# Kernel tuning notes

Hardware: AMD Instinct MI355X
Metric: run time of the kernel (lower is better)

## Reference

```python
import jax, jax.numpy as jnp
import numpy as np

B, T, D_IN, H, OUT = 512, 512, 64, 256, 64
EPS = 1e-5


def _ln(x, w, b):
    m = x.mean(-1, keepdims=True)
    v = ((x - m) ** 2).mean(-1, keepdims=True)
    return (x - m) / jnp.sqrt(v + EPS) * w + b


def _cell(x, h_prev, Wg, bg, gnw, gnb, Wc, bc, cnw, cnb):
    # LayerNormGRU cell
    combined = jnp.concatenate([x, h_prev], axis=-1)          # [B, D+H]
    rz = _ln(combined @ Wg.T + bg, gnw, gnb)                  # [B, 2H]
    r, z = jnp.split(rz, 2, axis=-1)
    r, z = jax.nn.sigmoid(r), jax.nn.sigmoid(z)
    combined_r = jnp.concatenate([x, r * h_prev], axis=-1)
    n = jnp.tanh(_ln(combined_r @ Wc.T + bc, cnw, cnb))       # [B, H]
    return (1.0 - z) * h_prev + z * n


def setup_inputs() -> dict:
    key = jax.random.key(0)
    ks = jax.random.split(key, 24)

    def uni(k, shape, fan_in):
        lim = 1.0 / np.sqrt(fan_in)
        return jax.random.uniform(k, shape, jnp.float32, -lim, lim)

    d0 = D_IN + H   # layer 0 cell input width
    d1 = H + H      # layer 1 cell input width
    return {
        "x": jax.random.normal(ks[0], (B, T, D_IN), jnp.float32),
        # layer 0
        "Wg0": uni(ks[1], (2 * H, d0), d0), "bg0": uni(ks[2], (2 * H,), d0),
        "gnw0": jnp.ones((2 * H,), jnp.float32), "gnb0": jnp.zeros((2 * H,), jnp.float32),
        "Wc0": uni(ks[3], (H, d0), d0), "bc0": uni(ks[4], (H,), d0),
        "cnw0": jnp.ones((H,), jnp.float32), "cnb0": jnp.zeros((H,), jnp.float32),
        # layer 1
        "Wg1": uni(ks[5], (2 * H, d1), d1), "bg1": uni(ks[6], (2 * H,), d1),
        "gnw1": jnp.ones((2 * H,), jnp.float32), "gnb1": jnp.zeros((2 * H,), jnp.float32),
        "Wc1": uni(ks[7], (H, d1), d1), "bc1": uni(ks[8], (H,), d1),
        "cnw1": jnp.ones((H,), jnp.float32), "cnb1": jnp.zeros((H,), jnp.float32),
        # output head
        "fcW": uni(ks[9], (OUT, H), H), "fcb": uni(ks[10], (OUT,), H),
    }


def reference(x, Wg0, bg0, gnw0, gnb0, Wc0, bc0, cnw0, cnb0,
              Wg1, bg1, gnw1, gnb1, Wc1, bc1, cnw1, cnb1, fcW, fcb):
    b = x.shape[0]
    h_init = (jnp.zeros((b, H), x.dtype), jnp.zeros((b, H), x.dtype))

    def step(carry, xt):
        h0, h1 = carry
        h0 = _cell(xt, h0, Wg0, bg0, gnw0, gnb0, Wc0, bc0, cnw0, cnb0)
        h1 = _cell(h0, h1, Wg1, bg1, gnw1, gnb1, Wc1, bc1, cnw1, cnb1)
        return (h0, h1), None

    (h0, h1), _ = jax.lax.scan(step, h_init, jnp.swapaxes(x, 0, 1))  # scan over T
    return h1 @ fcW.T + fcb  # [B, OUT]
```

## Files before the change

### kernel.cpp

```cpp
#include <hip/hip_runtime.h>


#define B_   512
#define T_   512
#define DIN  64
#define H_   256
#define OUT_ 64
#define EPS_ 1e-5f

typedef __attribute__((ext_vector_type(8))) short bf16x8;
typedef __attribute__((ext_vector_type(4))) float f32x4;

__device__ __forceinline__ unsigned short f2bf(float f) {
  unsigned int u = __float_as_uint(f);
  u += 0x7fffu + ((u >> 16) & 1u);
  return (unsigned short)(u >> 16);
}
__device__ __forceinline__ float bfh(unsigned short u) {
  return __uint_as_float(((unsigned int)u) << 16);
}
__device__ __forceinline__ float sigm_(float x) {
  return __builtin_amdgcn_rcpf(1.f + __expf(-x));
}
__device__ __forceinline__ float tanh_(float x) {
  return 1.f - 2.f * __builtin_amdgcn_rcpf(__expf(2.f * x) + 1.f);
}
template<int C>
__device__ __forceinline__ float dpp_add(float v) {
  int r = __builtin_amdgcn_update_dpp(0, __float_as_int(v), C, 0xF, 0xF, false);
  return v + __int_as_float(r);
}
__device__ __forceinline__ float red16(float v) {
  v = dpp_add<0x121>(v);
  v = dpp_add<0x122>(v);
  v = dpp_add<0x124>(v);
  v = dpp_add<0x128>(v);
  return v;
}

#define PIN8A(a) asm volatile("" : "+a"(a[0]), "+a"(a[1]), "+a"(a[2]), "+a"(a[3]), \
                                   "+a"(a[4]), "+a"(a[5]), "+a"(a[6]), "+a"(a[7]))

__global__ void prep_frag(const float* __restrict__ w, unsigned short* __restrict__ dst,
                          int N, int Ksrc, int koff) {
  int gid = blockIdx.x * 256 + threadIdx.x;
  if (gid >= N * 256) return;
  int n = gid >> 8, k = gid & 255;
  int idx = (((n >> 4) * 8 + (k >> 5)) * 64 + ((n & 15) + 16 * ((k >> 3) & 3))) * 8 + (k & 7);
  dst[idx] = f2bf(w[(size_t)n * Ksrc + koff + k]);
}

__global__ void prep_wx(const float* __restrict__ wg, const float* __restrict__ wc,
                        unsigned short* __restrict__ dst, int KX, int Kg, int Kc) {
  int gid = blockIdx.x * 256 + threadIdx.x;
  if (gid >= 768 * KX) return;
  int n = gid / KX, k = gid - n * KX;
  float v = (n < 512) ? wg[(size_t)n * Kg + k] : wc[(size_t)(n - 512) * Kc + k];
  dst[gid] = f2bf(v);
}

__global__ void bias_cat(const float* __restrict__ bg, const float* __restrict__ bc,
                         float* __restrict__ dst) {
  int i = blockIdx.x * 256 + threadIdx.x;
  if (i < 768) dst[i] = (i < 512) ? bg[i] : bc[i - 512];
}

__device__ __forceinline__ void precomp_tile(
    const void* __restrict__ Asrc, const unsigned short* __restrict__ wx,
    const float* __restrict__ bias, unsigned short* __restrict__ Pc,
    int TC, int t0, int KX, int AFP32,
    int mi, int nb, unsigned short* A_s, unsigned short* B_s, int t256)
{
  const int lane = t256 & 63, wv = t256 >> 6;
  const int m0 = mi * 128;
  const int bt = m0 / (TC * 16);
  const int tt0 = (m0 - bt * TC * 16) >> 4;
  const int mq = wv >> 1, nq = wv & 1;
  const int crow0 = (lane >> 4) * 4;

  f32x4 acc[4][4];
#pragma unroll
  for (int i = 0; i < 4; ++i)
#pragma unroll
    for (int j = 0; j < 4; ++j) acc[i][j] = (f32x4){0, 0, 0, 0};

  for (int kb = 0; kb < (KX >> 6); ++kb) {
    __syncthreads();
#pragma unroll
    for (int it = 0; it < 4; ++it) {
      int s = t256 + it * 256;
      int rg = s >> 3, k8 = s & 7;
      int mt = rg >> 4, r15 = rg & 15;
      int dl = r15 + 16 * (k8 & 3), kc = k8 >> 2;
      if (AFP32) {
        const float* xp = (const float*)Asrc +
            (((size_t)(bt * 16 + r15)) * T_ + (t0 + tt0 + mt)) * DIN + kb * 64 + k8 * 8;
        float4 u0 = *(const float4*)xp, u1 = *(const float4*)(xp + 4);
        unsigned short tmp[8];
        tmp[0] = f2bf(u0.x); tmp[1] = f2bf(u0.y); tmp[2] = f2bf(u0.z); tmp[3] = f2bf(u0.w);
        tmp[4] = f2bf(u1.x); tmp[5] = f2bf(u1.y); tmp[6] = f2bf(u1.z); tmp[7] = f2bf(u1.w);
        *reinterpret_cast<bf16x8*>(&A_s[((mt * 2 + kc) * 64 + dl) * 8]) =
            *reinterpret_cast<bf16x8*>(tmp);
      } else {
        const unsigned short* ap = (const unsigned short*)Asrc +
            ((size_t)(m0 + rg)) * KX + kb * 64 + k8 * 8;
        *reinterpret_cast<bf16x8*>(&A_s[((mt * 2 + kc) * 64 + dl) * 8]) =
            *reinterpret_cast<const bf16x8*>(ap);
      }
      const unsigned short* bp = wx + ((size_t)(nb + rg)) * KX + kb * 64 + k8 * 8;
      *reinterpret_cast<bf16x8*>(&B_s[((mt * 2 + kc) * 64 + dl) * 8]) =
          *reinterpret_cast<const bf16x8*>(bp);
    }
    __syncthreads();
#pragma unroll
    for (int kc = 0; kc < 2; ++kc) {
      bf16x8 av[4], bv[4];
#pragma unroll
      for (int i = 0; i < 4; ++i) {
        av[i] = *reinterpret_cast<const bf16x8*>(&A_s[(((mq * 4 + i) * 2 + kc) * 64 + lane) * 8]);
        bv[i] = *reinterpret_cast<const bf16x8*>(&B_s[(((nq * 4 + i) * 2 + kc) * 64 + lane) * 8]);
      }
#pragma unroll
      for (int i = 0; i < 4; ++i)
#pragma unroll
        for (int j = 0; j < 4; ++j)
          acc[i][j] = __builtin_amdgcn_mfma_f32_16x16x32_bf16(av[i], bv[j], acc[i][j], 0, 0, 0);
    }
  }
  float bb[4];
#pragma unroll
  for (int j = 0; j < 4; ++j) bb[j] = bias[nb + nq * 64 + j * 16 + (lane & 15)];
#pragma unroll
  for (int i = 0; i < 4; ++i) {
    int tt = tt0 + mq * 4 + i;
#pragma unroll
    for (int j = 0; j < 4; ++j) {
      int n = nb + nq * 64 + j * 16 + (lane & 15);
      ushort4 o;
      o.x = f2bf(acc[i][j][0] + bb[j]); o.y = f2bf(acc[i][j][1] + bb[j]);
      o.z = f2bf(acc[i][j][2] + bb[j]); o.w = f2bf(acc[i][j][3] + bb[j]);
      *reinterpret_cast<ushort4*>(&Pc[((size_t)(bt * TC + tt) * 768 + n) * 16 + crow0]) = o;
    }
  }
}

__launch_bounds__(256)
__global__ void precomp_std(const void* __restrict__ Asrc,
                            const unsigned short* __restrict__ wx,
                            const float* __restrict__ bias,
                            unsigned short* __restrict__ Pc,
                            int TC, int t0, int KX, int AFP32) {
  __shared__ __align__(16) unsigned short A_s[8192];
  __shared__ __align__(16) unsigned short B_s[8192];
  precomp_tile(Asrc, wx, bias, Pc, TC, t0, KX, AFP32,
               blockIdx.x, blockIdx.y * 128, A_s, B_s, threadIdx.x);
}

__device__ __forceinline__ void gru_body(
    unsigned char* smem, int bt,
    const unsigned short* __restrict__ gfrag,
    const unsigned short* __restrict__ cfrag,
    const unsigned short* __restrict__ Pc,
    const float* __restrict__ gnw, const float* __restrict__ gnb,
    const float* __restrict__ cnw, const float* __restrict__ cnb,
    float* __restrict__ hstate, unsigned short* __restrict__ h0out,
    int TC, int first)
{
  unsigned short* wc_s = (unsigned short*)smem;
  unsigned short (*h_s)[264]  = (unsigned short(*)[264])(smem + 131072);
  unsigned short (*rh_s)[264] = (unsigned short(*)[264])(smem + 139520);
  float (*sumP)[20] = (float(*)[20])(smem + 147968);
  float (*sqP)[20]  = (float(*)[20])(smem + 148608);
  float2* mnrs = (float2*)(smem + 149248);

  const int tid = threadIdx.x, lane = tid & 63, wv = tid >> 6;
  const int b0 = bt * 16;
  const int arow = lane & 15, koff = (lane >> 4) * 8, crow0 = (lane >> 4) * 4;
  const int colr0 = 32 * wv + (lane & 15), colr1 = colr0 + 16;
  const int nt0 = 2 * wv, nt1 = 2 * wv + 1, nt2 = 16 + 2 * wv, nt3 = 17 + 2 * wv;

  for (int i = tid; i < 8192; i += 512)
    *reinterpret_cast<bf16x8*>(&wc_s[i * 8]) = *reinterpret_cast<const bf16x8*>(&cfrag[i * 8]);

  bf16x8 wgr0[8], wgr1[8], wgr2[8], wgr3[8];
#pragma unroll
  for (int kc = 0; kc < 8; ++kc) {
    wgr0[kc] = *reinterpret_cast<const bf16x8*>(&gfrag[((nt0 * 8 + kc) * 64 + lane) * 8]);
    wgr1[kc] = *reinterpret_cast<const bf16x8*>(&gfrag[((nt1 * 8 + kc) * 64 + lane) * 8]);
    wgr2[kc] = *reinterpret_cast<const bf16x8*>(&gfrag[((nt2 * 8 + kc) * 64 + lane) * 8]);
    wgr3[kc] = *reinterpret_cast<const bf16x8*>(&gfrag[((nt3 * 8 + kc) * 64 + lane) * 8]);
  }

  const float gw_r0 = gnw[colr0], gb_r0 = gnb[colr0];
  const float gw_r1 = gnw[colr1], gb_r1 = gnb[colr1];
  const float gw_z0 = gnw[256 + colr0], gb_z0 = gnb[256 + colr0];
  const float gw_z1 = gnw[256 + colr1], gb_z1 = gnb[256 + colr1];
  const float cw0 = cnw[colr0], cb0 = cnb[colr0];
  const float cw1 = cnw[colr1], cb1 = cnb[colr1];

  float hm[2][4];
  if (first) {
#pragma unroll
    for (int g = 0; g < 4; ++g) { hm[0][g] = 0.f; hm[1][g] = 0.f; }
    for (int i = tid; i < 16 * 264; i += 512) (&h_s[0][0])[i] = 0;
  } else {
#pragma unroll
    for (int g = 0; g < 4; ++g) {
      hm[0][g] = hstate[(size_t)(b0 + crow0 + g) * 256 + colr0];
      hm[1][g] = hstate[(size_t)(b0 + crow0 + g) * 256 + colr1];
    }
    int r = tid >> 5, c8 = (tid & 31) * 8;
    float4 v0 = *reinterpret_cast<const float4*>(&hstate[(size_t)(b0 + r) * 256 + c8]);
    float4 v1 = *reinterpret_cast<const float4*>(&hstate[(size_t)(b0 + r) * 256 + c8 + 4]);
    ushort4 o0, o1;
    o0.x = f2bf(v0.x); o0.y = f2bf(v0.y); o0.z = f2bf(v0.z); o0.w = f2bf(v0.w);
    o1.x = f2bf(v1.x); o1.y = f2bf(v1.y); o1.z = f2bf(v1.z); o1.w = f2bf(v1.w);
    *reinterpret_cast<ushort4*>(&h_s[r][c8]) = o0;
    *reinterpret_cast<ushort4*>(&h_s[r][c8 + 4]) = o1;
  }
  __syncthreads();

  const unsigned short* Pr0 = Pc + ((size_t)bt * TC * 768 + colr0) * 16;

  for (int tt = 0; tt < TC; ++tt) {
    PIN8A(wgr0); PIN8A(wgr1); PIN8A(wgr2); PIN8A(wgr3);

    ushort4 pr0 = *reinterpret_cast<const ushort4*>(Pr0 + crow0);
    ushort4 pr1 = *reinterpret_cast<const ushort4*>(Pr0 + 16 * 16 + crow0);
    ushort4 pz0 = *reinterpret_cast<const ushort4*>(Pr0 + 256 * 16 + crow0);
    ushort4 pz1 = *reinterpret_cast<const ushort4*>(Pr0 + 272 * 16 + crow0);
    ushort4 pn0 = *reinterpret_cast<const ushort4*>(Pr0 + 512 * 16 + crow0);
    ushort4 pn1 = *reinterpret_cast<const ushort4*>(Pr0 + 528 * 16 + crow0);
    Pr0 += 12288;

    f32x4 a0 = {0, 0, 0, 0}, a1 = {0, 0, 0, 0}, a2 = {0, 0, 0, 0}, a3 = {0, 0, 0, 0};
#pragma unroll
    for (int kc = 0; kc < 8; ++kc) {
      bf16x8 av = *reinterpret_cast<const bf16x8*>(&h_s[arow][kc * 32 + koff]);
      a0 = __builtin_amdgcn_mfma_f32_16x16x32_bf16(av, wgr0[kc], a0, 0, 0, 0);
      a1 = __builtin_amdgcn_mfma_f32_16x16x32_bf16(av, wgr1[kc], a1, 0, 0, 0);
      a2 = __builtin_amdgcn_mfma_f32_16x16x32_bf16(av, wgr2[kc], a2, 0, 0, 0);
      a3 = __builtin_amdgcn_mfma_f32_16x16x32_bf16(av, wgr3[kc], a3, 0, 0, 0);
    }
    float vr0[4], vr1[4], vz0[4], vz1[4];
    {
      float s4[4], q4[4];
#pragma unroll
      for (int g = 0; g < 4; ++g) {
        vr0[g] = a0[g] + bfh(((const unsigned short*)&pr0)[g]);
        vr1[g] = a1[g] + bfh(((const unsigned short*)&pr1)[g]);
        vz0[g] = a2[g] + bfh(((const unsigned short*)&pz0)[g]);
        vz1[g] = a3[g] + bfh(((const unsigned short*)&pz1)[g]);
        s4[g] = red16(vr0[g] + vr1[g] + vz0[g] + vz1[g]);
        q4[g] = red16(vr0[g] * vr0[g] + vr1[g] * vr1[g] + vz0[g] * vz0[g] + vz1[g] * vz1[g]);
      }
      if ((lane & 15) == 0) {
        *reinterpret_cast<f32x4*>(&sumP[wv][crow0]) = (f32x4){s4[0], s4[1], s4[2], s4[3]};
        *reinterpret_cast<f32x4*>(&sqP[wv][crow0])  = (f32x4){q4[0], q4[1], q4[2], q4[3]};
      }
    }
    __syncthreads();

    {
      int sg = lane >> 4, rr = lane & 15;
      float S = sumP[2 * sg][rr] + sumP[2 * sg + 1][rr];
      float Q = sqP[2 * sg][rr] + sqP[2 * sg + 1][rr];
      S += __shfl_xor(S, 16, 64); Q += __shfl_xor(Q, 16, 64);
      S += __shfl_xor(S, 32, 64); Q += __shfl_xor(Q, 32, 64);
      float mn = S * (1.f / 512.f);
      float rs = __builtin_amdgcn_rsqf(Q * (1.f / 512.f) - mn * mn + EPS_);
      if (lane < 16) mnrs[lane] = make_float2(mn, rs);
    }
    float zf[2][4];
#pragma unroll
    for (int g = 0; g < 4; ++g) {
      float2 mr = mnrs[crow0 + g];
      float rv0 = sigm_(fmaf((vr0[g] - mr.x) * mr.y, gw_r0, gb_r0));
      float rv1 = sigm_(fmaf((vr1[g] - mr.x) * mr.y, gw_r1, gb_r1));
      zf[0][g]  = sigm_(fmaf((vz0[g] - mr.x) * mr.y, gw_z0, gb_z0));
      zf[1][g]  = sigm_(fmaf((vz1[g] - mr.x) * mr.y, gw_z1, gb_z1));
      rh_s[crow0 + g][colr0] = f2bf(rv0 * hm[0][g]);
      rh_s[crow0 + g][colr1] = f2bf(rv1 * hm[1][g]);
    }
    __syncthreads();

    f32x4 c0a = {0, 0, 0, 0}, c1a = {0, 0, 0, 0};
#pragma unroll
    for (int kc = 0; kc < 8; ++kc) {
      bf16x8 av = *reinterpret_cast<const bf16x8*>(&rh_s[arow][kc * 32 + koff]);
      bf16x8 b0v = *reinterpret_cast<const bf16x8*>(&wc_s[((nt0 * 8 + kc) * 64 + lane) * 8]);
      bf16x8 b1v = *reinterpret_cast<const bf16x8*>(&wc_s[((nt1 * 8 + kc) * 64 + lane) * 8]);
      c0a = __builtin_amdgcn_mfma_f32_16x16x32_bf16(av, b0v, c0a, 0, 0, 0);
      c1a = __builtin_amdgcn_mfma_f32_16x16x32_bf16(av, b1v, c1a, 0, 0, 0);
    }
    float vc0[4], vc1[4];
    {
      float s4[4], q4[4];
#pragma unroll
      for (int g = 0; g < 4; ++g) {
        vc0[g] = c0a[g] + bfh(((const unsigned short*)&pn0)[g]);
        vc1[g] = c1a[g] + bfh(((const unsigned short*)&pn1)[g]);
        s4[g] = red16(vc0[g] + vc1[g]);
        q4[g] = red16(vc0[g] * vc0[g] + vc1[g] * vc1[g]);
      }
      if ((lane & 15) == 0) {
        *reinterpret_cast<f32x4*>(&sumP[wv][crow0]) = (f32x4){s4[0], s4[1], s4[2], s4[3]};
        *reinterpret_cast<f32x4*>(&sqP[wv][crow0])  = (f32x4){q4[0], q4[1], q4[2], q4[3]};
      }
    }
    __syncthreads();

    {
      int sg = lane >> 4, rr = lane & 15;
      float S = sumP[2 * sg][rr] + sumP[2 * sg + 1][rr];
      float Q = sqP[2 * sg][rr] + sqP[2 * sg + 1][rr];
      S += __shfl_xor(S, 16, 64); Q += __shfl_xor(Q, 16, 64);
      S += __shfl_xor(S, 32, 64); Q += __shfl_xor(Q, 32, 64);
      float mn = S * (1.f / 256.f);
      float rs = __builtin_amdgcn_rsqf(Q * (1.f / 256.f) - mn * mn + EPS_);
      if (lane < 16) mnrs[lane] = make_float2(mn, rs);
    }
    unsigned short* hrow = h0out ? (h0out + (size_t)(bt * TC + tt) * 4096) : (unsigned short*)nullptr;
#pragma unroll
    for (int g = 0; g < 4; ++g) {
      float2 mr = mnrs[crow0 + g];
      float n0 = tanh_(fmaf((vc0[g] - mr.x) * mr.y, cw0, cb0));
      float n1 = tanh_(fmaf((vc1[g] - mr.x) * mr.y, cw1, cb1));
      float h0n = fmaf(zf[0][g], n0 - hm[0][g], hm[0][g]);
      float h1n = fmaf(zf[1][g], n1 - hm[1][g], hm[1][g]);
      hm[0][g] = h0n; hm[1][g] = h1n;
      unsigned short hb0 = f2bf(h0n), hb1 = f2bf(h1n);
      h_s[crow0 + g][colr0] = hb0;
      h_s[crow0 + g][colr1] = hb1;
      if (hrow) {
        hrow[(size_t)(crow0 + g) * 256 + colr0] = hb0;
        hrow[(size_t)(crow0 + g) * 256 + colr1] = hb1;
      }
    }
    __syncthreads();
  }

#pragma unroll
  for (int g = 0; g < 4; ++g) {
    hstate[(size_t)(b0 + crow0 + g) * 256 + colr0] = hm[0][g];
    hstate[(size_t)(b0 + crow0 + g) * 256 + colr1] = hm[1][g];
  }
}

__launch_bounds__(512, 2)
__global__ void mega(
    const float* __restrict__ x,
    const unsigned short* __restrict__ g0h, const unsigned short* __restrict__ c0h,
    const unsigned short* __restrict__ g1h, const unsigned short* __restrict__ c1h,
    const unsigned short* __restrict__ wx0, const unsigned short* __restrict__ wx1,
    const float* __restrict__ b768_0, const float* __restrict__ b768_1,
    const float* __restrict__ gnw0, const float* __restrict__ gnb0,
    const float* __restrict__ cnw0, const float* __restrict__ cnb0,
    const float* __restrict__ gnw1, const float* __restrict__ gnb1,
    const float* __restrict__ cnw1, const float* __restrict__ cnb1,
    float* __restrict__ hst0, float* __restrict__ hst1,
    unsigned short* __restrict__ P0a, unsigned short* __restrict__ P0b,
    unsigned short* __restrict__ P1a, unsigned short* __restrict__ P1b,
    unsigned short* __restrict__ h0a, unsigned short* __restrict__ h0b,
    int k, int TC, int NC)
{
  __shared__ __align__(16) unsigned char smem[149504];
  const int bid = blockIdx.x;

  if (bid < 32) {
    if (k >= NC) return;
    unsigned short* P0 = (k & 1) ? P0b : P0a;
    unsigned short* h0 = (k & 1) ? h0b : h0a;
    gru_body(smem, bid, g0h, c0h, P0, gnw0, gnb0, cnw0, cnb0, hst0, h0, TC, k == 0);
  } else if (bid < 64) {
    int kD = k - 2;
    if (kD < 0 || kD >= NC) return;
    unsigned short* P1 = (kD & 1) ? P1b : P1a;
    gru_body(smem, bid - 32, g1h, c1h, P1, gnw1, gnb1, cnw1, cnb1, hst1,
             (unsigned short*)nullptr, TC, kD == 0);
  } else if (bid < 160) {
    int kA = k + 1;
    if (kA >= NC) return;
    unsigned short* P0 = (kA & 1) ? P0b : P0a;
    int team = (bid - 64) * 2 + (threadIdx.x >> 8);
    int t256 = threadIdx.x & 255;
    unsigned short* A_s = (unsigned short*)(smem + (threadIdx.x >> 8) * 32768);
    unsigned short* B_s = A_s + 8192;
    int ntile = 24 * TC;
    for (int i = team; i < ntile; i += 192) {
      int mi = i % (4 * TC), ni = i / (4 * TC);
      precomp_tile(x, wx0, b768_0, P0, TC, kA * TC, 64, 1, mi, ni * 128, A_s, B_s, t256);
    }
  } else {
    int kC = k - 1;
    if (kC < 0 || kC >= NC) return;
    const unsigned short* h0 = (kC & 1) ? h0b : h0a;
    unsigned short* P1 = (kC & 1) ? P1b : P1a;
    int team = (bid - 160) * 2 + (threadIdx.x >> 8);
    int t256 = threadIdx.x & 255;
    unsigned short* A_s = (unsigned short*)(smem + (threadIdx.x >> 8) * 32768);
    unsigned short* B_s = A_s + 8192;
    int ntile = 24 * TC;
    for (int i = team; i < ntile; i += 192) {
      int mi = i % (4 * TC), ni = i / (4 * TC);
      precomp_tile(h0, wx1, b768_1, P1, TC, 0, 256, 0, mi, ni * 128, A_s, B_s, t256);
    }
  }
}

__launch_bounds__(256)
__global__ void head_k(const float* __restrict__ h1, const float* __restrict__ fcW,
                       const float* __restrict__ fcb, float* __restrict__ out) {
  __shared__ float hs[16][256];
  const int tid = threadIdx.x, b0 = blockIdx.x * 16;
  for (int i = tid; i < 16 * 64; i += 256) {
    int r = i >> 6, c4 = (i & 63) * 4;
    *reinterpret_cast<float4*>(&hs[r][c4]) =
        *reinterpret_cast<const float4*>(&h1[(size_t)(b0 + r) * 256 + c4]);
  }
  __syncthreads();
  int r = tid >> 4, o = (tid & 15) * 4;
  float a0 = fcb[o], a1 = fcb[o + 1], a2 = fcb[o + 2], a3 = fcb[o + 3];
  for (int k = 0; k < 256; ++k) {
    float h = hs[r][k];
    a0 = fmaf(h, fcW[(size_t)(o + 0) * 256 + k], a0);
    a1 = fmaf(h, fcW[(size_t)(o + 1) * 256 + k], a1);
    a2 = fmaf(h, fcW[(size_t)(o + 2) * 256 + k], a2);
    a3 = fmaf(h, fcW[(size_t)(o + 3) * 256 + k], a3);
  }
  float4 ov = {a0, a1, a2, a3};
  *reinterpret_cast<float4*>(&out[(size_t)(b0 + r) * 64 + o]) = ov;
}

extern "C" void kernel_launch(void* const* d_in, const int* in_sizes, int n_in,
                              void* d_out, int out_size, void* d_ws, size_t ws_size,
                              hipStream_t stream) {
  (void)in_sizes; (void)n_in; (void)out_size;
  const float* x    = (const float*)d_in[0];
  const float* Wg0  = (const float*)d_in[1];
  const float* bg0  = (const float*)d_in[2];
  const float* gnw0 = (const float*)d_in[3];
  const float* gnb0 = (const float*)d_in[4];
  const float* Wc0  = (const float*)d_in[5];
  const float* bc0  = (const float*)d_in[6];
  const float* cnw0 = (const float*)d_in[7];
  const float* cnb0 = (const float*)d_in[8];
  const float* Wg1  = (const float*)d_in[9];
  const float* bg1  = (const float*)d_in[10];
  const float* gnw1 = (const float*)d_in[11];
  const float* gnb1 = (const float*)d_in[12];
  const float* Wc1  = (const float*)d_in[13];
  const float* bc1  = (const float*)d_in[14];
  const float* cnw1 = (const float*)d_in[15];
  const float* cnb1 = (const float*)d_in[16];
  const float* fcW  = (const float*)d_in[17];
  const float* fcb  = (const float*)d_in[18];

  float* hst0 = (float*)d_ws;
  float* hst1 = hst0 + 131072;
  float* b768_0 = hst1 + 131072;
  float* b768_1 = b768_0 + 768;
  unsigned short* g0h = (unsigned short*)(b768_1 + 768);
  unsigned short* c0h = g0h + 131072;
  unsigned short* g1h = c0h + 65536;
  unsigned short* c1h = g1h + 131072;
  unsigned short* wx0 = c1h + 65536;
  unsigned short* wx1 = wx0 + 49152;
  unsigned short* dynbase = wx1 + 196608;

  const size_t fixed_bytes = (size_t)((char*)dynbase - (char*)d_ws);
  int TC = 32;
  while (TC > 4) {
    size_t need = fixed_bytes + (size_t)TC * 3670016;
    if (need <= ws_size) break;
    TC >>= 1;
  }
  const int NC = T_ / TC;

  unsigned short* P0a = dynbase;
  unsigned short* P0b = P0a + (size_t)TC * 393216;
  unsigned short* P1a = P0b + (size_t)TC * 393216;
  unsigned short* P1b = P1a + (size_t)TC * 393216;
  unsigned short* h0a = P1b + (size_t)TC * 393216;
  unsigned short* h0b = h0a + (size_t)TC * 131072;

  prep_frag<<<512, 256, 0, stream>>>(Wg0, g0h, 512, 320, 64);
  prep_frag<<<256, 256, 0, stream>>>(Wc0, c0h, 256, 320, 64);
  prep_frag<<<512, 256, 0, stream>>>(Wg1, g1h, 512, 512, 256);
  prep_frag<<<256, 256, 0, stream>>>(Wc1, c1h, 256, 512, 256);
  prep_wx<<<192, 256, 0, stream>>>(Wg0, Wc0, wx0, 64, 320, 320);
  prep_wx<<<768, 256, 0, stream>>>(Wg1, Wc1, wx1, 256, 512, 512);
  bias_cat<<<3, 256, 0, stream>>>(bg0, bc0, b768_0);
  bias_cat<<<3, 256, 0, stream>>>(bg1, bc1, b768_1);

  precomp_std<<<dim3(4 * TC, 6), 256, 0, stream>>>(x, wx0, b768_0, P0a, TC, 0, 64, 1);

  for (int k = 0; k < NC + 2; ++k) {
    mega<<<256, 512, 0, stream>>>(x, g0h, c0h, g1h, c1h, wx0, wx1, b768_0, b768_1,
        gnw0, gnb0, cnw0, cnb0, gnw1, gnb1, cnw1, cnb1,
        hst0, hst1, P0a, P0b, P1a, P1b, h0a, h0b, k, TC, NC);
  }

  head_k<<<32, 256, 0, stream>>>(hst1, fcW, fcb, (float*)d_out);
}
```

Measured before the change: 2.738 ms.

## Replace per-chunk kernel launches with a persistent cooperative kernel using grid sync

Replaces the host loop of NC+2 mega launches with one cooperative persistent kernel that steps through the chunks and separates them with grid.sync(). The GRU blocks now keep their gate weights in registers, the candidate weights in LDS and the hidden state in registers across chunks, so the per-chunk weight reload and the hstate round trip through global memory go away. The risk is the cost of grid-wide barriers, and a cooperative launch needs all 256 blocks co-resident at 512 threads with about 146 KB of LDS each. If the cooperative launch fails, the code falls back to the old multi-launch loop.

```diff
diff --git a/kernel.cpp b/kernel.cpp
--- a/kernel.cpp
+++ b/kernel.cpp
@@ -1,4 +1,7 @@
 #include <hip/hip_runtime.h>
+#include <hip/hip_cooperative_groups.h>
+
+namespace cg = cooperative_groups;
 
 
 #define B_   512
@@ -156,6 +159,202 @@
                blockIdx.x, blockIdx.y * 128, A_s, B_s, threadIdx.x);
 }
 
+struct GP {
+  float gw_r0, gb_r0, gw_r1, gb_r1;
+  float gw_z0, gb_z0, gw_z1, gb_z1;
+  float cw0, cb0, cw1, cb1;
+};
+
+__device__ __forceinline__ void gru_init(
+    unsigned char* smem,
+    const unsigned short* __restrict__ gfrag,
+    const unsigned short* __restrict__ cfrag,
+    const float* __restrict__ gnw, const float* __restrict__ gnb,
+    const float* __restrict__ cnw, const float* __restrict__ cnb,
+    bf16x8 (&wgr0)[8], bf16x8 (&wgr1)[8], bf16x8 (&wgr2)[8], bf16x8 (&wgr3)[8],
+    GP& p, float (&hm)[2][4])
+{
+  unsigned short* wc_s = (unsigned short*)smem;
+  unsigned short (*h_s)[264] = (unsigned short(*)[264])(smem + 131072);
+  const int tid = threadIdx.x, lane = tid & 63, wv = tid >> 6;
+  const int colr0 = 32 * wv + (lane & 15), colr1 = colr0 + 16;
+  const int nt0 = 2 * wv, nt1 = 2 * wv + 1, nt2 = 16 + 2 * wv, nt3 = 17 + 2 * wv;
+
+  for (int i = tid; i < 8192; i += 512)
+    *reinterpret_cast<bf16x8*>(&wc_s[i * 8]) = *reinterpret_cast<const bf16x8*>(&cfrag[i * 8]);
+#pragma unroll
+  for (int kc = 0; kc < 8; ++kc) {
+    wgr0[kc] = *reinterpret_cast<const bf16x8*>(&gfrag[((nt0 * 8 + kc) * 64 + lane) * 8]);
+    wgr1[kc] = *reinterpret_cast<const bf16x8*>(&gfrag[((nt1 * 8 + kc) * 64 + lane) * 8]);
+    wgr2[kc] = *reinterpret_cast<const bf16x8*>(&gfrag[((nt2 * 8 + kc) * 64 + lane) * 8]);
+    wgr3[kc] = *reinterpret_cast<const bf16x8*>(&gfrag[((nt3 * 8 + kc) * 64 + lane) * 8]);
+  }
+  p.gw_r0 = gnw[colr0];       p.gb_r0 = gnb[colr0];
+  p.gw_r1 = gnw[colr1];       p.gb_r1 = gnb[colr1];
+  p.gw_z0 = gnw[256 + colr0]; p.gb_z0 = gnb[256 + colr0];
+  p.gw_z1 = gnw[256 + colr1]; p.gb_z1 = gnb[256 + colr1];
+  p.cw0 = cnw[colr0]; p.cb0 = cnb[colr0];
+  p.cw1 = cnw[colr1]; p.cb1 = cnb[colr1];
+#pragma unroll
+  for (int g = 0; g < 4; ++g) { hm[0][g] = 0.f; hm[1][g] = 0.f; }
+  for (int i = tid; i < 16 * 264; i += 512) (&h_s[0][0])[i] = 0;
+  __syncthreads();
+}
+
+__device__ __forceinline__ void gru_chunk(
+    unsigned char* smem, int bt,
+    bf16x8 (&wgr0)[8], bf16x8 (&wgr1)[8], bf16x8 (&wgr2)[8], bf16x8 (&wgr3)[8],
+    const GP& p, float (&hm)[2][4],
+    const unsigned short* __restrict__ Pc,
+    unsigned short* __restrict__ h0out,
+    int TC)
+{
+  unsigned short* wc_s = (unsigned short*)smem;
+  unsigned short (*h_s)[264]  = (unsigned short(*)[264])(smem + 131072);
+  unsigned short (*rh_s)[264] = (unsigned short(*)[264])(smem + 139520);
+  float (*sumP)[20] = (float(*)[20])(smem + 147968);
+  float (*sqP)[20]  = (float(*)[20])(smem + 148608);
+  float2* mnrs = (float2*)(smem + 149248);
+
+  const int tid = threadIdx.x, lane = tid & 63, wv = tid >> 6;
+  const int arow = lane & 15, koff = (lane >> 4) * 8, crow0 = (lane >> 4) * 4;
+  const int colr0 = 32 * wv + (lane & 15), colr1 = colr0 + 16;
+  const int nt0 = 2 * wv, nt1 = 2 * wv + 1;
+
+  const unsigned short* Pr0 = Pc + ((size_t)bt * TC * 768 + colr0) * 16;
+
+  for (int tt = 0; tt < TC; ++tt) {
+    PIN8A(wgr0); PIN8A(wgr1); PIN8A(wgr2); PIN8A(wgr3);
+
+    ushort4 pr0 = *reinterpret_cast<const ushort4*>(Pr0 + crow0);
+    ushort4 pr1 = *reinterpret_cast<const ushort4*>(Pr0 + 16 * 16 + crow0);
+    ushort4 pz0 = *reinterpret_cast<const ushort4*>(Pr0 + 256 * 16 + crow0);
+    ushort4 pz1 = *reinterpret_cast<const ushort4*>(Pr0 + 272 * 16 + crow0);
+    ushort4 pn0 = *reinterpret_cast<const ushort4*>(Pr0 + 512 * 16 + crow0);
+    ushort4 pn1 = *reinterpret_cast<const ushort4*>(Pr0 + 528 * 16 + crow0);
+    Pr0 += 12288;
+
+    f32x4 a0 = {0, 0, 0, 0}, a1 = {0, 0, 0, 0}, a2 = {0, 0, 0, 0}, a3 = {0, 0, 0, 0};
+#pragma unroll
+    for (int kc = 0; kc < 8; ++kc) {
+      bf16x8 av = *reinterpret_cast<const bf16x8*>(&h_s[arow][kc * 32 + koff]);
+      a0 = __builtin_amdgcn_mfma_f32_16x16x32_bf16(av, wgr0[kc], a0, 0, 0, 0);
+      a1 = __builtin_amdgcn_mfma_f32_16x16x32_bf16(av, wgr1[kc], a1, 0, 0, 0);
+      a2 = __builtin_amdgcn_mfma_f32_16x16x32_bf16(av, wgr2[kc], a2, 0, 0, 0);
+      a3 = __builtin_amdgcn_mfma_f32_16x16x32_bf16(av, wgr3[kc], a3, 0, 0, 0);
+    }
+    float vr0[4], vr1[4], vz0[4], vz1[4];
+    {
+      float s4[4], q4[4];
+#pragma unroll
+      for (int g = 0; g < 4; ++g) {
+        vr0[g] = a0[g] + bfh(((const unsigned short*)&pr0)[g]);
+        vr1[g] = a1[g] + bfh(((const unsigned short*)&pr1)[g]);
+        vz0[g] = a2[g] + bfh(((const unsigned short*)&pz0)[g]);
+        vz1[g] = a3[g] + bfh(((const unsigned short*)&pz1)[g]);
+        s4[g] = red16(vr0[g] + vr1[g] + vz0[g] + vz1[g]);
+        q4[g] = red16(vr0[g] * vr0[g] + vr1[g] * vr1[g] + vz0[g] * vz0[g] + vz1[g] * vz1[g]);
+      }
+      if ((lane & 15) == 0) {
+        *reinterpret_cast<f32x4*>(&sumP[wv][crow0]) = (f32x4){s4[0], s4[1], s4[2], s4[3]};
+        *reinterpret_cast<f32x4*>(&sqP[wv][crow0])  = (f32x4){q4[0], q4[1], q4[2], q4[3]};
+      }
+    }
+    __syncthreads();
+
+    {
+      int sg = lane >> 4, rr = lane & 15;
+      float S = sumP[2 * sg][rr] + sumP[2 * sg + 1][rr];
+      float Q = sqP[2 * sg][rr] + sqP[2 * sg + 1][rr];
+      S += __shfl_xor(S, 16, 64); Q += __shfl_xor(Q, 16, 64);
+      S += __shfl_xor(S, 32, 64); Q += __shfl_xor(Q, 32, 64);
+      float mn = S * (1.f / 512.f);
+      float rs = __builtin_amdgcn_rsqf(Q * (1.f / 512.f) - mn * mn + EPS_);
+      if (lane < 16) mnrs[lane] = make_float2(mn, rs);
+    }
+    float zf[2][4];
+#pragma unroll
+    for (int g = 0; g < 4; ++g) {
+      float2 mr = mnrs[crow0 + g];
+      float rv0 = sigm_(fmaf((vr0[g] - mr.x) * mr.y, p.gw_r0, p.gb_r0));
+      float rv1 = sigm_(fmaf((vr1[g] - mr.x) * mr.y, p.gw_r1, p.gb_r1));
+      zf[0][g]  = sigm_(fmaf((vz0[g] - mr.x) * mr.y, p.gw_z0, p.gb_z0));
+      zf[1][g]  = sigm_(fmaf((vz1[g] - mr.x) * mr.y, p.gw_z1, p.gb_z1));
+      rh_s[crow0 + g][colr0] = f2bf(rv0 * hm[0][g]);
+      rh_s[crow0 + g][colr1] = f2bf(rv1 * hm[1][g]);
+    }
+    __syncthreads();
+
+    f32x4 c0a = {0, 0, 0, 0}, c1a = {0, 0, 0, 0};
+#pragma unroll
+    for (int kc = 0; kc < 8; ++kc) {
+      bf16x8 av = *reinterpret_cast<const bf16x8*>(&rh_s[arow][kc * 32 + koff]);
+      bf16x8 b0v = *reinterpret_cast<const bf16x8*>(&wc_s[((nt0 * 8 + kc) * 64 + lane) * 8]);
+      bf16x8 b1v = *reinterpret_cast<const bf16x8*>(&wc_s[((nt1 * 8 + kc) * 64 + lane) * 8]);
+      c0a = __builtin_amdgcn_mfma_f32_16x16x32_bf16(av, b0v, c0a, 0, 0, 0);
+      c1a = __builtin_amdgcn_mfma_f32_16x16x32_bf16(av, b1v, c1a, 0, 0, 0);
+    }
+    float vc0[4], vc1[4];
+    {
+      float s4[4], q4[4];
+#pragma unroll
+      for (int g = 0; g < 4; ++g) {
+        vc0[g] = c0a[g] + bfh(((const unsigned short*)&pn0)[g]);
+        vc1[g] = c1a[g] + bfh(((const unsigned short*)&pn1)[g]);
+        s4[g] = red16(vc0[g] + vc1[g]);
+        q4[g] = red16(vc0[g] * vc0[g] + vc1[g] * vc1[g]);
+      }
+      if ((lane & 15) == 0) {
+        *reinterpret_cast<f32x4*>(&sumP[wv][crow0]) = (f32x4){s4[0], s4[1], s4[2], s4[3]};
+        *reinterpret_cast<f32x4*>(&sqP[wv][crow0])  = (f32x4){q4[0], q4[1], q4[2], q4[3]};
+      }
+    }
+    __syncthreads();
+
+    {
+      int sg = lane >> 4, rr = lane & 15;
+      float S = sumP[2 * sg][rr] + sumP[2 * sg + 1][rr];
+      float Q = sqP[2 * sg][rr] + sqP[2 * sg + 1][rr];
+      S += __shfl_xor(S, 16, 64); Q += __shfl_xor(Q, 16, 64);
+      S += __shfl_xor(S, 32, 64); Q += __shfl_xor(Q, 32, 64);
+      float mn = S * (1.f / 256.f);
+      float rs = __builtin_amdgcn_rsqf(Q * (1.f / 256.f) - mn * mn + EPS_);
+      if (lane < 16) mnrs[lane] = make_float2(mn, rs);
+    }
+    unsigned short* hrow = h0out ? (h0out + (size_t)(bt * TC + tt) * 4096) : (unsigned short*)nullptr;
+#pragma unroll
+    for (int g = 0; g < 4; ++g) {
+      float2 mr = mnrs[crow0 + g];
+      float n0 = tanh_(fmaf((vc0[g] - mr.x) * mr.y, p.cw0, p.cb0));
+      float n1 = tanh_(fmaf((vc1[g] - mr.x) * mr.y, p.cw1, p.cb1));
+      float h0n = fmaf(zf[0][g], n0 - hm[0][g], hm[0][g]);
+      float h1n = fmaf(zf[1][g], n1 - hm[1][g], hm[1][g]);
+      hm[0][g] = h0n; hm[1][g] = h1n;
+      unsigned short hb0 = f2bf(h0n), hb1 = f2bf(h1n);
+      h_s[crow0 + g][colr0] = hb0;
+      h_s[crow0 + g][colr1] = hb1;
+      if (hrow) {
+        hrow[(size_t)(crow0 + g) * 256 + colr0] = hb0;
+        hrow[(size_t)(crow0 + g) * 256 + colr1] = hb1;
+      }
+    }
+    __syncthreads();
+  }
+}
+
+__device__ __forceinline__ void gru_store(float* __restrict__ hstate, int bt,
+                                          float (&hm)[2][4]) {
+  const int lane = threadIdx.x & 63, wv = threadIdx.x >> 6;
+  const int crow0 = (lane >> 4) * 4;
+  const int colr0 = 32 * wv + (lane & 15), colr1 = colr0 + 16;
+  const int b0 = bt * 16;
+#pragma unroll
+  for (int g = 0; g < 4; ++g) {
+    hstate[(size_t)(b0 + crow0 + g) * 256 + colr0] = hm[0][g];
+    hstate[(size_t)(b0 + crow0 + g) * 256 + colr1] = hm[1][g];
+  }
+}
+
 __device__ __forceinline__ void gru_body(
     unsigned char* smem, int bt,
     const unsigned short* __restrict__ gfrag,
@@ -166,44 +365,15 @@
     float* __restrict__ hstate, unsigned short* __restrict__ h0out,
     int TC, int first)
 {
-  unsigned short* wc_s = (unsigned short*)smem;
-  unsigned short (*h_s)[264]  = (unsigned short(*)[264])(smem + 131072);
-  unsigned short (*rh_s)[264] = (unsigned short(*)[264])(smem + 139520);
-  float (*sumP)[20] = (float(*)[20])(smem + 147968);
-  float (*sqP)[20]  = (float(*)[20])(smem + 148608);
-  float2* mnrs = (float2*)(smem + 149248);
-
-  const int tid = threadIdx.x, lane = tid & 63, wv = tid >> 6;
-  const int b0 = bt * 16;
-  const int arow = lane & 15, koff = (lane >> 4) * 8, crow0 = (lane >> 4) * 4;
-  const int colr0 = 32 * wv + (lane & 15), colr1 = colr0 + 16;
-  const int nt0 = 2 * wv, nt1 = 2 * wv + 1, nt2 = 16 + 2 * wv, nt3 = 17 + 2 * wv;
-
-  for (int i = tid; i < 8192; i += 512)
-    *reinterpret_cast<bf16x8*>(&wc_s[i * 8]) = *reinterpret_cast<const bf16x8*>(&cfrag[i * 8]);
-
   bf16x8 wgr0[8], wgr1[8], wgr2[8], wgr3[8];
-#pragma unroll
-  for (int kc = 0; kc < 8; ++kc) {
-    wgr0[kc] = *reinterpret_cast<const bf16x8*>(&gfrag[((nt0 * 8 + kc) * 64 + lane) * 8]);
-    wgr1[kc] = *reinterpret_cast<const bf16x8*>(&gfrag[((nt1 * 8 + kc) * 64 + lane) * 8]);
-    wgr2[kc] = *reinterpret_cast<const bf16x8*>(&gfrag[((nt2 * 8 + kc) * 64 + lane) * 8]);
-    wgr3[kc] = *reinterpret_cast<const bf16x8*>(&gfrag[((nt3 * 8 + kc) * 64 + lane) * 8]);
-  }
-
-  const float gw_r0 = gnw[colr0], gb_r0 = gnb[colr0];
-  const float gw_r1 = gnw[colr1], gb_r1 = gnb[colr1];
-  const float gw_z0 = gnw[256 + colr0], gb_z0 = gnb[256 + colr0];
-  const float gw_z1 = gnw[256 + colr1], gb_z1 = gnb[256 + colr1];
-  const float cw0 = cnw[colr0], cb0 = cnb[colr0];
-  const float cw1 = cnw[colr1], cb1 = cnb[colr1];
-
-  float hm[2][4];
-  if (first) {
-#pragma unroll
-    for (int g = 0; g < 4; ++g) { hm[0][g] = 0.f; hm[1][g] = 0.f; }
-    for (int i = tid; i < 16 * 264; i += 512) (&h_s[0][0])[i] = 0;
-  } else {
+  GP p; float hm[2][4];
+  gru_init(smem, gfrag, cfrag, gnw, gnb, cnw, cnb, wgr0, wgr1, wgr2, wgr3, p, hm);
+  if (!first) {
+    unsigned short (*h_s)[264] = (unsigned short(*)[264])(smem + 131072);
+    const int tid = threadIdx.x, lane = tid & 63, wv = tid >> 6;
+    const int crow0 = (lane >> 4) * 4;
+    const int colr0 = 32 * wv + (lane & 15), colr1 = colr0 + 16;
+    const int b0 = bt * 16;
 #pragma unroll
     for (int g = 0; g < 4; ++g) {
       hm[0][g] = hstate[(size_t)(b0 + crow0 + g) * 256 + colr0];
@@ -217,171 +387,115 @@
     o1.x = f2bf(v1.x); o1.y = f2bf(v1.y); o1.z = f2bf(v1.z); o1.w = f2bf(v1.w);
     *reinterpret_cast<ushort4*>(&h_s[r][c8]) = o0;
     *reinterpret_cast<ushort4*>(&h_s[r][c8 + 4]) = o1;
-  }
-  __syncthreads();
-
-  const unsigned short* Pr0 = Pc + ((size_t)bt * TC * 768 + colr0) * 16;
-
-  for (int tt = 0; tt < TC; ++tt) {
-    PIN8A(wgr0); PIN8A(wgr1); PIN8A(wgr2); PIN8A(wgr3);
-
-    ushort4 pr0 = *reinterpret_cast<const ushort4*>(Pr0 + crow0);
-    ushort4 pr1 = *reinterpret_cast<const ushort4*>(Pr0 + 16 * 16 + crow0);
-    ushort4 pz0 = *reinterpret_cast<const ushort4*>(Pr0 + 256 * 16 + crow0);
-    ushort4 pz1 = *reinterpret_cast<const ushort4*>(Pr0 + 272 * 16 + crow0);
-    ushort4 pn0 = *reinterpret_cast<const ushort4*>(Pr0 + 512 * 16 + crow0);
-    ushort4 pn1 = *reinterpret_cast<const ushort4*>(Pr0 + 528 * 16 + crow0);
-    Pr0 += 12288;
-
-    f32x4 a0 = {0, 0, 0, 0}, a1 = {0, 0, 0, 0}, a2 = {0, 0, 0, 0}, a3 = {0, 0, 0, 0};
-#pragma unroll
-    for (int kc = 0; kc < 8; ++kc) {
-      bf16x8 av = *reinterpret_cast<const bf16x8*>(&h_s[arow][kc * 32 + koff]);
-      a0 = __builtin_amdgcn_mfma_f32_16x16x32_bf16(av, wgr0[kc], a0, 0, 0, 0);
-      a1 = __builtin_amdgcn_mfma_f32_16x16x32_bf16(av, wgr1[kc], a1, 0, 0, 0);
-      a2 = __builtin_amdgcn_mfma_f32_16x16x32_bf16(av, wgr2[kc], a2, 0, 0, 0);
-      a3 = __builtin_amdgcn_mfma_f32_16x16x32_bf16(av, wgr3[kc], a3, 0, 0, 0);
-    }
-    float vr0[4], vr1[4], vz0[4], vz1[4];
-    {
-      float s4[4], q4[4];
-#pragma unroll
-      for (int g = 0; g < 4; ++g) {
-        vr0[g] = a0[g] + bfh(((const unsigned short*)&pr0)[g]);
-        vr1[g] = a1[g] + bfh(((const unsigned short*)&pr1)[g]);
-        vz0[g] = a2[g] + bfh(((const unsigned short*)&pz0)[g]);
-        vz1[g] = a3[g] + bfh(((const unsigned short*)&pz1)[g]);
-        s4[g] = red16(vr0[g] + vr1[g] + vz0[g] + vz1[g]);
-        q4[g] = red16(vr0[g] * vr0[g] + vr1[g] * vr1[g] + vz0[g] * vz0[g] + vz1[g] * vz1[g]);
-      }
-      if ((lane & 15) == 0) {
-        *reinterpret_cast<f32x4*>(&sumP[wv][crow0]) = (f32x4){s4[0], s4[1], s4[2], s4[3]};
-        *reinterpret_cast<f32x4*>(&sqP[wv][crow0])  = (f32x4){q4[0], q4[1], q4[2], q4[3]};
-      }
-    }
     __syncthreads();
-
-    {
-      int sg = lane >> 4, rr = lane & 15;
-      float S = sumP[2 * sg][rr] + sumP[2 * sg + 1][rr];
-      float Q = sqP[2 * sg][rr] + sqP[2 * sg + 1][rr];
-      S += __shfl_xor(S, 16, 64); Q += __shfl_xor(Q, 16, 64);
-      S += __shfl_xor(S, 32, 64); Q += __shfl_xor(Q, 32, 64);
-      float mn = S * (1.f / 512.f);
-      float rs = __builtin_amdgcn_rsqf(Q * (1.f / 512.f) - mn * mn + EPS_);
-      if (lane < 16) mnrs[lane] = make_float2(mn, rs);
-    }
-    float zf[2][4];
-#pragma unroll
-    for (int g = 0; g < 4; ++g) {
-      float2 mr = mnrs[crow0 + g];
-      float rv0 = sigm_(fmaf((vr0[g] - mr.x) * mr.y, gw_r0, gb_r0));
-      float rv1 = sigm_(fmaf((vr1[g] - mr.x) * mr.y, gw_r1, gb_r1));
-      zf[0][g]  = sigm_(fmaf((vz0[g] - mr.x) * mr.y, gw_z0, gb_z0));
-      zf[1][g]  = sigm_(fmaf((vz1[g] - mr.x) * mr.y, gw_z1, gb_z1));
-      rh_s[crow0 + g][colr0] = f2bf(rv0 * hm[0][g]);
-      rh_s[crow0 + g][colr1] = f2bf(rv1 * hm[1][g]);
-    }
-    __syncthreads();
-
-    f32x4 c0a = {0, 0, 0, 0}, c1a = {0, 0, 0, 0};
-#pragma unroll
-    for (int kc = 0; kc < 8; ++kc) {
-      bf16x8 av = *reinterpret_cast<const bf16x8*>(&rh_s[arow][kc * 32 + koff]);
-      bf16x8 b0v = *reinterpret_cast<const bf16x8*>(&wc_s[((nt0 * 8 + kc) * 64 + lane) * 8]);
-      bf16x8 b1v = *reinterpret_cast<const bf16x8*>(&wc_s[((nt1 * 8 + kc) * 64 + lane) * 8]);
-      c0a = __builtin_amdgcn_mfma_f32_16x16x32_bf16(av, b0v, c0a, 0, 0, 0);
-      c1a = __builtin_amdgcn_mfma_f32_16x16x32_bf16(av, b1v, c1a, 0, 0, 0);
-    }
-    float vc0[4], vc1[4];
-    {
-      float s4[4], q4[4];
-#pragma unroll
-      for (int g = 0; g < 4; ++g) {
-        vc0[g] = c0a[g] + bfh(((const unsigned short*)&pn0)[g]);
-        vc1[g] = c1a[g] + bfh(((const unsigned short*)&pn1)[g]);
-        s4[g] = red16(vc0[g] + vc1[g]);
-        q4[g] = red16(vc0[g] * vc0[g] + vc1[g] * vc1[g]);
-      }
-      if ((lane & 15) == 0) {
-        *reinterpret_cast<f32x4*>(&sumP[wv][crow0]) = (f32x4){s4[0], s4[1], s4[2], s4[3]};
-        *reinterpret_cast<f32x4*>(&sqP[wv][crow0])  = (f32x4){q4[0], q4[1], q4[2], q4[3]};
-      }
-    }
-    __syncthreads();
-
-    {
-      int sg = lane >> 4, rr = lane & 15;
-      float S = sumP[2 * sg][rr] + sumP[2 * sg + 1][rr];
-      float Q = sqP[2 * sg][rr] + sqP[2 * sg + 1][rr];
-      S += __shfl_xor(S, 16, 64); Q += __shfl_xor(Q, 16, 64);
-      S += __shfl_xor(S, 32, 64); Q += __shfl_xor(Q, 32, 64);
-      float mn = S * (1.f / 256.f);
-      float rs = __builtin_amdgcn_rsqf(Q * (1.f / 256.f) - mn * mn + EPS_);
-      if (lane < 16) mnrs[lane] = make_float2(mn, rs);
-    }
-    unsigned short* hrow = h0out ? (h0out + (size_t)(bt * TC + tt) * 4096) : (unsigned short*)nullptr;
-#pragma unroll
-    for (int g = 0; g < 4; ++g) {
-      float2 mr = mnrs[crow0 + g];
-      float n0 = tanh_(fmaf((vc0[g] - mr.x) * mr.y, cw0, cb0));
-      float n1 = tanh_(fmaf((vc1[g] - mr.x) * mr.y, cw1, cb1));
-      float h0n = fmaf(zf[0][g], n0 - hm[0][g], hm[0][g]);
-      float h1n = fmaf(zf[1][g], n1 - hm[1][g], hm[1][g]);
-      hm[0][g] = h0n; hm[1][g] = h1n;
-      unsigned short hb0 = f2bf(h0n), hb1 = f2bf(h1n);
-      h_s[crow0 + g][colr0] = hb0;
-      h_s[crow0 + g][colr1] = hb1;
-      if (hrow) {
-        hrow[(size_t)(crow0 + g) * 256 + colr0] = hb0;
-        hrow[(size_t)(crow0 + g) * 256 + colr1] = hb1;
-      }
-    }
-    __syncthreads();
-  }
-
-#pragma unroll
-  for (int g = 0; g < 4; ++g) {
-    hstate[(size_t)(b0 + crow0 + g) * 256 + colr0] = hm[0][g];
-    hstate[(size_t)(b0 + crow0 + g) * 256 + colr1] = hm[1][g];
-  }
-}
+  }
+  gru_chunk(smem, bt, wgr0, wgr1, wgr2, wgr3, p, hm, Pc, h0out, TC);
+  gru_store(hstate, bt, hm);
+}
+
+struct PArgs {
+  const float* x;
+  const unsigned short *g0h, *c0h, *g1h, *c1h, *wx0, *wx1;
+  const float *b768_0, *b768_1;
+  const float *gnw0, *gnb0, *cnw0, *cnb0, *gnw1, *gnb1, *cnw1, *cnb1;
+  float *hst0, *hst1;
+  unsigned short *P0a, *P0b, *P1a, *P1b, *h0a, *h0b;
+  int TC, NC;
+};
 
 __launch_bounds__(512, 2)
-__global__ void mega(
-    const float* __restrict__ x,
-    const unsigned short* __restrict__ g0h, const unsigned short* __restrict__ c0h,
-    const unsigned short* __restrict__ g1h, const unsigned short* __restrict__ c1h,
-    const unsigned short* __restrict__ wx0, const unsigned short* __restrict__ wx1,
-    const float* __restrict__ b768_0, const float* __restrict__ b768_1,
-    const float* __restrict__ gnw0, const float* __restrict__ gnb0,
-    const float* __restrict__ cnw0, const float* __restrict__ cnb0,
-    const float* __restrict__ gnw1, const float* __restrict__ gnb1,
-    const float* __restrict__ cnw1, const float* __restrict__ cnb1,
-    float* __restrict__ hst0, float* __restrict__ hst1,
-    unsigned short* __restrict__ P0a, unsigned short* __restrict__ P0b,
-    unsigned short* __restrict__ P1a, unsigned short* __restrict__ P1b,
-    unsigned short* __restrict__ h0a, unsigned short* __restrict__ h0b,
-    int k, int TC, int NC)
-{
+__global__ void mega_persist(PArgs a) {
+  cg::grid_group grid = cg::this_grid();
   __shared__ __align__(16) unsigned char smem[149504];
   const int bid = blockIdx.x;
+  const int TC = a.TC, NC = a.NC;
+
+  if (bid < 64) {
+    const bool isB = bid < 32;
+    const int bt = isB ? bid : (bid - 32);
+    bf16x8 wgr0[8], wgr1[8], wgr2[8], wgr3[8];
+    GP p; float hm[2][4];
+    gru_init(smem,
+             isB ? a.g0h : a.g1h, isB ? a.c0h : a.c1h,
+             isB ? a.gnw0 : a.gnw1, isB ? a.gnb0 : a.gnb1,
+             isB ? a.cnw0 : a.cnw1, isB ? a.cnb0 : a.cnb1,
+             wgr0, wgr1, wgr2, wgr3, p, hm);
+    for (int k = 0; k < NC + 2; ++k) {
+      int myk = isB ? k : (k - 2);
+      if (myk >= 0 && myk < NC) {
+        const unsigned short* Pc = isB ? ((myk & 1) ? a.P0b : a.P0a)
+                                       : ((myk & 1) ? a.P1b : a.P1a);
+        unsigned short* h0o = isB ? ((myk & 1) ? a.h0b : a.h0a)
+                                  : (unsigned short*)nullptr;
+        gru_chunk(smem, bt, wgr0, wgr1, wgr2, wgr3, p, hm, Pc, h0o, TC);
+      }
+      __threadfence();
+      grid.sync();
+    }
+    if (!isB) gru_store(a.hst1, bt, hm);
+  } else if (bid < 160) {
+    for (int k = 0; k < NC + 2; ++k) {
+      int kA = k + 1;
+      if (kA < NC) {
+        unsigned short* P0 = (kA & 1) ? a.P0b : a.P0a;
+        int team = (bid - 64) * 2 + (threadIdx.x >> 8);
+        int t256 = threadIdx.x & 255;
+        unsigned short* A_s = (unsigned short*)(smem + (threadIdx.x >> 8) * 32768);
+        unsigned short* B_s = A_s + 8192;
+        int ntile = 24 * TC;
+        for (int i = team; i < ntile; i += 192) {
+          int mi = i % (4 * TC), ni = i / (4 * TC);
+          precomp_tile(a.x, a.wx0, a.b768_0, P0, TC, kA * TC, 64, 1,
+                       mi, ni * 128, A_s, B_s, t256);
+        }
+      }
+      __threadfence();
+      grid.sync();
+    }
+  } else {
+    for (int k = 0; k < NC + 2; ++k) {
+      int kC = k - 1;
+      if (kC >= 0 && kC < NC) {
+        const unsigned short* h0 = (kC & 1) ? a.h0b : a.h0a;
+        unsigned short* P1 = (kC & 1) ? a.P1b : a.P1a;
+        int team = (bid - 160) * 2 + (threadIdx.x >> 8);
+        int t256 = threadIdx.x & 255;
+        unsigned short* A_s = (unsigned short*)(smem + (threadIdx.x >> 8) * 32768);
+        unsigned short* B_s = A_s + 8192;
+        int ntile = 24 * TC;
+        for (int i = team; i < ntile; i += 192) {
+          int mi = i % (4 * TC), ni = i / (4 * TC);
+          precomp_tile(h0, a.wx1, a.b768_1, P1, TC, 0, 256, 0,
+                       mi, ni * 128, A_s, B_s, t256);
+        }
+      }
+      __threadfence();
+      grid.sync();
+    }
+  }
+}
+
+__launch_bounds__(512, 2)
+__global__ void mega(PArgs a, int k) {
+  __shared__ __align__(16) unsigned char smem[149504];
+  const int bid = blockIdx.x;
+  const int TC = a.TC, NC = a.NC;
 
   if (bid < 32) {
     if (k >= NC) return;
-    unsigned short* P0 = (k & 1) ? P0b : P0a;
-    unsigned short* h0 = (k & 1) ? h0b : h0a;
-    gru_body(smem, bid, g0h, c0h, P0, gnw0, gnb0, cnw0, cnb0, hst0, h0, TC, k == 0);
+    gru_body(smem, bid, a.g0h, a.c0h, (k & 1) ? a.P0b : a.P0a,
+             a.gnw0, a.gnb0, a.cnw0, a.cnb0, a.hst0,
+             (k & 1) ? a.h0b : a.h0a, TC, k == 0);
   } else if (bid < 64) {
     int kD = k - 2;
     if (kD < 0 || kD >= NC) return;
-    unsigned short* P1 = (kD & 1) ? P1b : P1a;
-    gru_body(smem, bid - 32, g1h, c1h, P1, gnw1, gnb1, cnw1, cnb1, hst1,
+    gru_body(smem, bid - 32, a.g1h, a.c1h, (kD & 1) ? a.P1b : a.P1a,
+             a.gnw1, a.gnb1, a.cnw1, a.cnb1, a.hst1,
              (unsigned short*)nullptr, TC, kD == 0);
   } else if (bid < 160) {
     int kA = k + 1;
     if (kA >= NC) return;
-    unsigned short* P0 = (kA & 1) ? P0b : P0a;
+    unsigned short* P0 = (kA & 1) ? a.P0b : a.P0a;
     int team = (bid - 64) * 2 + (threadIdx.x >> 8);
     int t256 = threadIdx.x & 255;
     unsigned short* A_s = (unsigned short*)(smem + (threadIdx.x >> 8) * 32768);
@@ -389,13 +503,14 @@
     int ntile = 24 * TC;
     for (int i = team; i < ntile; i += 192) {
       int mi = i % (4 * TC), ni = i / (4 * TC);
-      precomp_tile(x, wx0, b768_0, P0, TC, kA * TC, 64, 1, mi, ni * 128, A_s, B_s, t256);
+      precomp_tile(a.x, a.wx0, a.b768_0, P0, TC, kA * TC, 64, 1,
+                   mi, ni * 128, A_s, B_s, t256);
     }
   } else {
     int kC = k - 1;
     if (kC < 0 || kC >= NC) return;
-    const unsigned short* h0 = (kC & 1) ? h0b : h0a;
-    unsigned short* P1 = (kC & 1) ? P1b : P1a;
+    const unsigned short* h0 = (kC & 1) ? a.h0b : a.h0a;
+    unsigned short* P1 = (kC & 1) ? a.P1b : a.P1a;
     int team = (bid - 160) * 2 + (threadIdx.x >> 8);
     int t256 = threadIdx.x & 255;
     unsigned short* A_s = (unsigned short*)(smem + (threadIdx.x >> 8) * 32768);
@@ -403,7 +518,8 @@
     int ntile = 24 * TC;
     for (int i = team; i < ntile; i += 192) {
       int mi = i % (4 * TC), ni = i / (4 * TC);
-      precomp_tile(h0, wx1, b768_1, P1, TC, 0, 256, 0, mi, ni * 128, A_s, B_s, t256);
+      precomp_tile(h0, a.wx1, a.b768_1, P1, TC, 0, 256, 0,
+                   mi, ni * 128, A_s, B_s, t256);
     }
   }
 }
@@ -495,10 +611,24 @@
 
   precomp_std<<<dim3(4 * TC, 6), 256, 0, stream>>>(x, wx0, b768_0, P0a, TC, 0, 64, 1);
 
-  for (int k = 0; k < NC + 2; ++k) {
-    mega<<<256, 512, 0, stream>>>(x, g0h, c0h, g1h, c1h, wx0, wx1, b768_0, b768_1,
-        gnw0, gnb0, cnw0, cnb0, gnw1, gnb1, cnw1, cnb1,
-        hst0, hst1, P0a, P0b, P1a, P1b, h0a, h0b, k, TC, NC);
+  PArgs pa;
+  pa.x = x;
+  pa.g0h = g0h; pa.c0h = c0h; pa.g1h = g1h; pa.c1h = c1h;
+  pa.wx0 = wx0; pa.wx1 = wx1;
+  pa.b768_0 = b768_0; pa.b768_1 = b768_1;
+  pa.gnw0 = gnw0; pa.gnb0 = gnb0; pa.cnw0 = cnw0; pa.cnb0 = cnb0;
+  pa.gnw1 = gnw1; pa.gnb1 = gnb1; pa.cnw1 = cnw1; pa.cnb1 = cnb1;
+  pa.hst0 = hst0; pa.hst1 = hst1;
+  pa.P0a = P0a; pa.P0b = P0b; pa.P1a = P1a; pa.P1b = P1b;
+  pa.h0a = h0a; pa.h0b = h0b;
+  pa.TC = TC; pa.NC = NC;
+
+  void* kargs[] = { (void*)&pa };
+  hipError_t ce = hipLaunchCooperativeKernel((const void*)mega_persist,
+                                             dim3(256), dim3(512), kargs, 0, stream);
+  if (ce != hipSuccess) {
+    for (int k = 0; k < NC + 2; ++k)
+      mega<<<256, 512, 0, stream>>>(pa, k);
   }
 
   head_k<<<32, 256, 0, stream>>>(hst1, fcW, fcb, (float*)d_out);
```

After: 3.517 ms. 1.28x slower.
